# Performance work log

Hardware: AMD Instinct MI355X
Metric: run time of the kernel (lower is better)

## Reference

```python
import jax, jax.numpy as jnp
import numpy as np

B, T, C, H = 4, 2048, 1024, 16


def setup_inputs() -> dict:
    key = jax.random.key(0)
    ks = jax.random.split(key, 5)
    s_attn = 1.0 / np.sqrt(C)
    s_proj = 1.0 / np.sqrt(C)
    return {
        "x": jax.random.normal(ks[0], (B, T, C), dtype=jnp.float32),
        "w_attn": jax.random.uniform(ks[1], (3 * C, C), dtype=jnp.float32, minval=-s_attn, maxval=s_attn),
        "b_attn": jax.random.uniform(ks[2], (3 * C,), dtype=jnp.float32, minval=-s_attn, maxval=s_attn),
        "w_proj": jax.random.uniform(ks[3], (C, C), dtype=jnp.float32, minval=-s_proj, maxval=s_proj),
        "b_proj": jax.random.uniform(ks[4], (C,), dtype=jnp.float32, minval=-s_proj, maxval=s_proj),
    }


def reference(x, w_attn, b_attn, w_proj, b_proj):
    b, t, c = x.shape
    hd = c // H  # head dim
    qkv = jnp.einsum('btc,dc->btd', x, w_attn) + b_attn  # [B,T,3C]
    q, k, v = jnp.split(qkv, 3, axis=-1)
    # [B,H,T,hd]
    q = q.reshape(b, t, H, hd).transpose(0, 2, 1, 3)
    k = k.reshape(b, t, H, hd).transpose(0, 2, 1, 3)
    v = v.reshape(b, t, H, hd).transpose(0, 2, 1, 3)
    att = jnp.einsum('bhqd,bhkd->bhqk', q, k) * (1.0 / np.sqrt(hd))
    mask = jnp.tril(jnp.ones((t, t), dtype=bool))  # causal
    att = jnp.where(mask, att, -jnp.inf)
    att = jax.nn.softmax(att, axis=-1)
    y = jnp.einsum('bhqk,bhkd->bhqd', att, v)
    y = y.transpose(0, 2, 1, 3).reshape(b, t, c)
    return jnp.einsum('btc,dc->btd', y, w_proj) + b_proj
```

## Files before the change

### kernel.cpp

```cpp
#include <hip/hip_runtime.h>

#define Bb 4
#define Tt 2048
#define Cc 1024
#define Hh 16
#define NQKV 3072
#define Mtot 8192

typedef __bf16 bf16_t;
typedef unsigned short u16;
typedef __bf16 bf16x8 __attribute__((ext_vector_type(8)));
typedef __bf16 bf16x4 __attribute__((ext_vector_type(4)));
typedef short short4v __attribute__((ext_vector_type(4)));
typedef float f32x4 __attribute__((ext_vector_type(4)));
typedef float f32x16 __attribute__((ext_vector_type(16)));
typedef unsigned uint2v __attribute__((ext_vector_type(2)));

union bfu { bf16_t b; u16 u; };
union trpair { short4v h[2]; bf16x8 v; };
union pfu { unsigned u[4]; bf16x8 v; };

#define QSCALE 0.18033688011112042f

#define TRD(dst, addr, OFF)                                                     \
  asm volatile("ds_read_b64_tr_b16 %0, %1 offset:" OFF                          \
               : "=v"(dst) : "v"(addr) : "memory")

__device__ __forceinline__ unsigned cvtpk(float a, float b) {
  unsigned r;
  asm("v_cvt_pk_bf16_f32 %0, %1, %2" : "=v"(r) : "v"(a), "v"(b));
  return r;
}
__device__ __forceinline__ uint2v plswap(unsigned a, unsigned b) {
  return __builtin_amdgcn_permlane32_swap(a, b, false, false);
}

#define GLOAD16(gsrc, ldst)                                                     \
  __builtin_amdgcn_global_load_lds(                                             \
      (const __attribute__((address_space(1))) unsigned int*)(gsrc),            \
      (__attribute__((address_space(3))) unsigned int*)(ldst), 16, 0, 0)

__device__ __forceinline__ void cvt8(const float* s, u16* d, size_t i, float f) {
  float4 a = *(const float4*)(s + i);
  float4 b = *(const float4*)(s + i + 4);
  bf16x8 v;
  v[0]=(bf16_t)(a.x*f); v[1]=(bf16_t)(a.y*f); v[2]=(bf16_t)(a.z*f); v[3]=(bf16_t)(a.w*f);
  v[4]=(bf16_t)(b.x*f); v[5]=(bf16_t)(b.y*f); v[6]=(bf16_t)(b.z*f); v[7]=(bf16_t)(b.w*f);
  *(bf16x8*)(d + i) = v;
}

__global__ __launch_bounds__(256) void cvt_all(
    const float* __restrict__ x, const float* __restrict__ w_attn,
    const float* __restrict__ w_proj, const float* __restrict__ b_attn,
    u16* __restrict__ xb, u16* __restrict__ wab, u16* __restrict__ wpb,
    float* __restrict__ sbias)
{
  const int blk = blockIdx.x;
  if (blk < 4096) {
    size_t i = ((size_t)blk * 256 + threadIdx.x) * 8;
    cvt8(x, xb, i, 1.0f);
  } else if (blk < 5632) {
    size_t i = ((size_t)(blk - 4096) * 256 + threadIdx.x) * 8;
    cvt8(w_attn, wab, i, (i < (size_t)Cc * Cc) ? QSCALE : 1.0f);
  } else if (blk < 6144) {
    size_t i = ((size_t)(blk - 5632) * 256 + threadIdx.x) * 8;
    cvt8(w_proj, wpb, i, 1.0f);
  } else {
    int i0 = (blk - 6144) * 2048 + threadIdx.x * 8;
#pragma unroll
    for (int j = 0; j < 8; ++j) {
      int i = i0 + j;
      if (i < NQKV) sbias[i] = b_attn[i] * ((i < Cc) ? QSCALE : 1.0f);
    }
  }
}

__global__ __launch_bounds__(512, 2) void gemm256(
    const u16* __restrict__ A, const u16* __restrict__ Bm,
    const float* __restrict__ bias, u16* __restrict__ Cout,
    int M, int N, int K)
{
  __shared__ __attribute__((aligned(16))) u16 sa[2][8192];
  __shared__ __attribute__((aligned(16))) u16 sb[2][8192];

  const int tid  = threadIdx.x;
  const int lane = tid & 63;
  const int w    = tid >> 6;
  const int wm   = w >> 2;
  const int wn   = w & 3;
  const int l15  = lane & 15;
  const int lh   = lane >> 4;
  const int bm   = blockIdx.x * 256;
  const int bn   = blockIdx.y * 256;

  f32x4 acc[8][4] = {};

  const int sr = tid >> 2;
  const int sc = (tid & 3) * 8;
  const u16* pa0 = A  + (size_t)(bm + sr) * K + sc;
  const u16* pa1 = A  + (size_t)(bm + 128 + sr) * K + sc;
  const u16* pb0 = Bm + (size_t)(bn + sr) * K + sc;
  const u16* pb1 = Bm + (size_t)(bn + 128 + sr) * K + sc;
  const int d0 = tid * 8;

#define STAGE_T(t, p) do {                                                      \
    GLOAD16(pa0 + (size_t)(t) * 32, &sa[p][d0]);                                \
    GLOAD16(pa1 + (size_t)(t) * 32, &sa[p][d0 + 4096]);                         \
    GLOAD16(pb0 + (size_t)(t) * 32, &sb[p][d0]);                                \
    GLOAD16(pb1 + (size_t)(t) * 32, &sb[p][d0 + 4096]);                         \
  } while (0)

  const int NT = K >> 5;
  STAGE_T(0, 0);
  STAGE_T(1, 1);

  for (int t = 0; t < NT; ++t) {
    const int p = t & 1;
    if (t + 1 < NT) asm volatile("s_waitcnt vmcnt(4)" ::: "memory");
    else            asm volatile("s_waitcnt vmcnt(0)" ::: "memory");
    __builtin_amdgcn_s_barrier();
    __builtin_amdgcn_sched_barrier(0);

    bf16x8 bfr[4], afr[8];
#pragma unroll
    for (int nf = 0; nf < 4; ++nf)
      bfr[nf] = *(const bf16x8*)&sb[p][(wn*64 + nf*16 + l15) * 32 + lh*8];
#pragma unroll
    for (int mf = 0; mf < 8; ++mf)
      afr[mf] = *(const bf16x8*)&sa[p][(wm*128 + mf*16 + l15) * 32 + lh*8];

    __builtin_amdgcn_s_setprio(1);
#pragma unroll
    for (int mf = 0; mf < 8; ++mf)
#pragma unroll
      for (int nf = 0; nf < 4; ++nf)
        acc[mf][nf] = __builtin_amdgcn_mfma_f32_16x16x32_bf16(
            afr[mf], bfr[nf], acc[mf][nf], 0, 0, 0);
    __builtin_amdgcn_s_setprio(0);
    __builtin_amdgcn_sched_barrier(0);
    __builtin_amdgcn_s_barrier();
    __builtin_amdgcn_sched_barrier(0);
    if (t + 2 < NT) STAGE_T(t + 2, p);
  }
#undef STAGE_T

#pragma unroll
  for (int mf = 0; mf < 8; ++mf)
#pragma unroll
    for (int nf = 0; nf < 4; ++nf) {
      const int col = bn + wn*64 + nf*16 + l15;
      const float bs = bias[col];
#pragma unroll
      for (int r = 0; r < 4; ++r) {
        const int row = bm + wm*128 + mf*16 + lh*4 + r;
        bfu cv; cv.b = (bf16_t)(acc[mf][nf][r] + bs);
        Cout[(size_t)row * N + col] = cv.u;
      }
    }
}

template <int OUTBF16>
__global__ __launch_bounds__(256) void gemm_bf16(
    const u16* __restrict__ A, const u16* __restrict__ Bm,
    const float* __restrict__ bias, void* __restrict__ Cout,
    int M, int N, int K)
{
  __shared__ __attribute__((aligned(16))) u16 sa[128][40];
  __shared__ __attribute__((aligned(16))) u16 sb[128][40];

  const int tid  = threadIdx.x;
  const int lane = tid & 63;
  const int wid  = tid >> 6;
  const int wr   = (wid >> 1) * 64;
  const int wc   = (wid & 1) * 64;
  const int l15  = lane & 15;
  const int lh   = lane >> 4;
  const int bm   = blockIdx.x * 128;
  const int bn   = blockIdx.y * 128;

  f32x4 acc[4][4] = {};

  const int srow = tid >> 1;
  const int sseg = (tid & 1) * 16;

  const u16* pa = A  + (size_t)(bm + srow) * K + sseg;
  const u16* pb = Bm + (size_t)(bn + srow) * K + sseg;

  uint4 ar0 = *(const uint4*)pa, ar1 = *(const uint4*)(pa + 8);
  uint4 br0 = *(const uint4*)pb, br1 = *(const uint4*)(pb + 8);
  pa += 32; pb += 32;

  for (int k0 = 0; k0 < K; k0 += 32) {
    __syncthreads();
    *(uint4*)&sa[srow][sseg]     = ar0;
    *(uint4*)&sa[srow][sseg + 8] = ar1;
    *(uint4*)&sb[srow][sseg]     = br0;
    *(uint4*)&sb[srow][sseg + 8] = br1;
    __syncthreads();
    if (k0 + 32 < K) {
      ar0 = *(const uint4*)pa; ar1 = *(const uint4*)(pa + 8);
      br0 = *(const uint4*)pb; br1 = *(const uint4*)(pb + 8);
      pa += 32; pb += 32;
    }
    bf16x8 af[4], bfv[4];
#pragma unroll
    for (int mi = 0; mi < 4; mi++)
      af[mi] = *(const bf16x8*)&sa[wr + mi*16 + l15][lh * 8];
#pragma unroll
    for (int ni = 0; ni < 4; ni++)
      bfv[ni] = *(const bf16x8*)&sb[wc + ni*16 + l15][lh * 8];
#pragma unroll
    for (int mi = 0; mi < 4; mi++)
#pragma unroll
      for (int ni = 0; ni < 4; ni++)
        acc[mi][ni] = __builtin_amdgcn_mfma_f32_16x16x32_bf16(
            af[mi], bfv[ni], acc[mi][ni], 0, 0, 0);
  }

#pragma unroll
  for (int mi = 0; mi < 4; mi++) {
#pragma unroll
    for (int ni = 0; ni < 4; ni++) {
      const int col = bn + wc + ni*16 + l15;
      const float bs = bias[col];
#pragma unroll
      for (int r = 0; r < 4; r++) {
        const int row = bm + wr + mi*16 + lh*4 + r;
        const float val = acc[mi][ni][r] + bs;
        if (OUTBF16) {
          bfu cv; cv.b = (bf16_t)val;
          ((u16*)Cout)[(size_t)row * N + col] = cv.u;
        } else {
          ((float*)Cout)[(size_t)row * N + col] = val;
        }
      }
    }
  }
}

#define BUFU 9216

__global__ __launch_bounds__(512) void attn_kernel(
    const u16* __restrict__ qkv, u16* __restrict__ y)
{
  __shared__ __attribute__((aligned(16))) u16 smem[3 * BUFU];

  const int tid  = threadIdx.x;
  const int lane = tid & 63;
  const int w    = tid >> 6;
  const int l31  = lane & 31;
  const int hh   = lane >> 5;
  const int l15  = lane & 15;
  const int lh   = lane >> 4;
  const int bh   = blockIdx.y;
  const int b    = bh >> 4;
  const int head = bh & 15;

  const size_t rowbase = (size_t)b * Tt * NQKV;

  const int skey = tid >> 3;
  const int sp   = tid & 7;
  const u16* kbase = qkv + rowbase + 1024 + head*64 + sp*8;
  const u16* vbase = qkv + rowbase + 2048 + head*64 + sp*8;

  const unsigned smemB = (unsigned)(size_t)(&smem[0]);
  const unsigned trl = smemB
      + ((lh>>1)*8 + (l15>>2))*144 + (lh&1)*32 + (l15&3)*8;

  uint4 kr0, vr0;
#define LOADREGS(t) do {                                                        \
    kr0 = *(const uint4*)(kbase + (size_t)((t)*64 + skey) * NQKV);              \
    vr0 = *(const uint4*)(vbase + (size_t)((t)*64 + skey) * NQKV);              \
  } while (0)
#define STAGEB(bofs) do {                                                       \
    *(uint4*)&smem[(bofs) + skey*72 + sp*8]        = kr0;                       \
    *(uint4*)&smem[(bofs) + 4608 + skey*72 + sp*8] = vr0;                       \
  } while (0)

  for (int half = 0; half < 2; ++half) {
    const int qx    = half ? (7 - (int)blockIdx.x) : (int)blockIdx.x;
    const int qbase = qx * 256;
    const int qw    = qbase + w * 32;
    const int qi    = qw + l31;
    const int ktiles = 4*qx + 4;

    bf16x8 qfrag[4];
#pragma unroll
    for (int m = 0; m < 4; ++m)
      qfrag[m] = *(const bf16x8*)(qkv + rowbase + (size_t)qi * NQKV
                                  + head*64 + m*16 + hh*8);

    f32x16 o0 = {}, o1 = {};
    float m_run = -1e30f, l_part = 0.0f;
    f32x16 sA0, sA1, sB0, sB1;

    auto qk = [&](f32x16& t0, f32x16& t1, int kofs, int kb0) {
      f32x16 a0 = {}, a1 = {};
      __builtin_amdgcn_s_setprio(1);
#pragma unroll
      for (int m = 0; m < 4; ++m) {
        const int co = m*16 + hh*8;
        bf16x8 k0 = *(const bf16x8*)&smem[kofs + l31*72 + co];
        bf16x8 k1 = *(const bf16x8*)&smem[kofs + (32 + l31)*72 + co];
        a0 = __builtin_amdgcn_mfma_f32_32x32x16_bf16(k0, qfrag[m], a0, 0,0,0);
        a1 = __builtin_amdgcn_mfma_f32_32x32x16_bf16(k1, qfrag[m], a1, 0,0,0);
      }
      __builtin_amdgcn_s_setprio(0);
      if (kb0 + 63 > qw) {
#pragma unroll
        for (int r = 0; r < 16; ++r) {
          const int crow = (r&3) + 8*(r>>2) + 4*hh;
          if (kb0 + crow > qi)      a0[r] = -1e30f;
          if (kb0 + 32 + crow > qi) a1[r] = -1e30f;
        }
      }
      t0 = a0; t1 = a1;
    };

    auto smpv = [&](f32x16& s0, f32x16& s1, int bofs) {
      float mx[8];
#pragma unroll
      for (int i = 0; i < 8; ++i)
        mx[i] = fmaxf(fmaxf(s0[i], s0[i+8]), fmaxf(s1[i], s1[i+8]));
#pragma unroll
      for (int i = 0; i < 4; ++i) mx[i] = fmaxf(mx[i], mx[i+4]);
      mx[0] = fmaxf(mx[0], mx[2]); mx[1] = fmaxf(mx[1], mx[3]);
      float rm = fmaxf(mx[0], mx[1]);
      {
        uint2v t = plswap(__float_as_uint(rm), __float_as_uint(rm));
        rm = fmaxf(__uint_as_float(t[0]), __uint_as_float(t[1]));
      }
      if (__any(rm > m_run + 8.0f)) {
        const float mn = fmaxf(m_run, rm);
        const float al = exp2f(m_run - mn);
        m_run = mn; l_part *= al;
#pragma unroll
        for (int r = 0; r < 16; ++r) { o0[r] *= al; o1[r] *= al; }
      }

      pfu pf0, pf1, pf2, pf3;
      float lp0 = 0.f, lp1 = 0.f, lp2 = 0.f, lp3 = 0.f;
      {
        float pe[16];
#pragma unroll
        for (int r = 0; r < 16; ++r) pe[r] = exp2f(s0[r] - m_run);
#pragma unroll
        for (int r = 0; r < 4; ++r) {
          lp0 += pe[r]; lp1 += pe[4+r]; lp2 += pe[8+r]; lp3 += pe[12+r];
        }
        unsigned a0 = cvtpk(pe[0],pe[1]),  a1 = cvtpk(pe[2],pe[3]);
        unsigned a2 = cvtpk(pe[4],pe[5]),  a3 = cvtpk(pe[6],pe[7]);
        uint2v x1 = plswap(a0, a2), x2 = plswap(a1, a3);
        pf0.u[0]=x1[0]; pf0.u[1]=x2[0]; pf0.u[2]=x1[1]; pf0.u[3]=x2[1];
        unsigned b0 = cvtpk(pe[8],pe[9]),  b1 = cvtpk(pe[10],pe[11]);
        unsigned b2 = cvtpk(pe[12],pe[13]), b3 = cvtpk(pe[14],pe[15]);
        uint2v x3 = plswap(b0, b2), x4 = plswap(b1, b3);
        pf1.u[0]=x3[0]; pf1.u[1]=x4[0]; pf1.u[2]=x3[1]; pf1.u[3]=x4[1];
      }
      {
        float pe[16];
#pragma unroll
        for (int r = 0; r < 16; ++r) pe[r] = exp2f(s1[r] - m_run);
#pragma unroll
        for (int r = 0; r < 4; ++r) {
          lp0 += pe[r]; lp1 += pe[4+r]; lp2 += pe[8+r]; lp3 += pe[12+r];
        }
        unsigned a0 = cvtpk(pe[0],pe[1]),  a1 = cvtpk(pe[2],pe[3]);
        unsigned a2 = cvtpk(pe[4],pe[5]),  a3 = cvtpk(pe[6],pe[7]);
        uint2v x1 = plswap(a0, a2), x2 = plswap(a1, a3);
        pf2.u[0]=x1[0]; pf2.u[1]=x2[0]; pf2.u[2]=x1[1]; pf2.u[3]=x2[1];
        unsigned b0 = cvtpk(pe[8],pe[9]),  b1 = cvtpk(pe[10],pe[11]);
        unsigned b2 = cvtpk(pe[12],pe[13]), b3 = cvtpk(pe[14],pe[15]);
        uint2v x3 = plswap(b0, b2), x4 = plswap(b1, b3);
        pf3.u[0]=x3[0]; pf3.u[1]=x4[0]; pf3.u[2]=x3[1]; pf3.u[3]=x4[1];
      }
      l_part += (lp0 + lp1) + (lp2 + lp3);

      const unsigned va = trl + (unsigned)(bofs*2 + 9216);
      short4v ta0,tb0,ta1,tb1,ta2,tb2,ta3,tb3,ta4,tb4,ta5,tb5,ta6,tb6,ta7,tb7;
      TRD(ta0, va, "0");    TRD(tb0, va, "576");
      TRD(ta1, va, "64");   TRD(tb1, va, "640");
      TRD(ta2, va, "2304"); TRD(tb2, va, "2880");
      TRD(ta3, va, "2368"); TRD(tb3, va, "2944");
      TRD(ta4, va, "4608"); TRD(tb4, va, "5184");
      TRD(ta5, va, "4672"); TRD(tb5, va, "5248");
      TRD(ta6, va, "6912"); TRD(tb6, va, "7488");
      TRD(ta7, va, "6976"); TRD(tb7, va, "7552");
      asm volatile("s_waitcnt lgkmcnt(0)" ::: "memory");
      __builtin_amdgcn_sched_barrier(0);
      trpair v00,v01,v10,v11,v20,v21,v30,v31;
      v00.h[0]=ta0; v00.h[1]=tb0;  v01.h[0]=ta1; v01.h[1]=tb1;
      v10.h[0]=ta2; v10.h[1]=tb2;  v11.h[0]=ta3; v11.h[1]=tb3;
      v20.h[0]=ta4; v20.h[1]=tb4;  v21.h[0]=ta5; v21.h[1]=tb5;
      v30.h[0]=ta6; v30.h[1]=tb6;  v31.h[0]=ta7; v31.h[1]=tb7;
      __builtin_amdgcn_s_setprio(1);
      o0 = __builtin_amdgcn_mfma_f32_32x32x16_bf16(v00.v, pf0.v, o0, 0,0,0);
      o1 = __builtin_amdgcn_mfma_f32_32x32x16_bf16(v01.v, pf0.v, o1, 0,0,0);
      o0 = __builtin_amdgcn_mfma_f32_32x32x16_bf16(v10.v, pf1.v, o0, 0,0,0);
      o1 = __builtin_amdgcn_mfma_f32_32x32x16_bf16(v11.v, pf1.v, o1, 0,0,0);
      o0 = __builtin_amdgcn_mfma_f32_32x32x16_bf16(v20.v, pf2.v, o0, 0,0,0);
      o1 = __builtin_amdgcn_mfma_f32_32x32x16_bf16(v21.v, pf2.v, o1, 0,0,0);
      o0 = __builtin_amdgcn_mfma_f32_32x32x16_bf16(v30.v, pf3.v, o0, 0,0,0);
      o1 = __builtin_amdgcn_mfma_f32_32x32x16_bf16(v31.v, pf3.v, o1, 0,0,0);
      __builtin_amdgcn_s_setprio(0);
    };

    LOADREGS(0);
    __syncthreads();
    STAGEB(0);
    LOADREGS(1);
    __syncthreads();
    qk(sA0, sA1, 0, 0);
    STAGEB(BUFU);
    LOADREGS(2);

    int cofs = 0, nofs = BUFU, fofs = 2*BUFU;

    for (int kt = 0; kt < ktiles; kt += 2) {
      __syncthreads();
      if ((kt+1)*64 <= qw + 31) qk(sB0, sB1, nofs, (kt+1)*64);
      if (kt*64 <= qw + 31)     smpv(sA0, sA1, cofs);
      if (kt + 2 < ktiles) {
        STAGEB(fofs);
        if (kt + 3 < ktiles) LOADREGS(kt + 3);
      }
      { int t = cofs; cofs = nofs; nofs = fofs; fofs = t; }

      __syncthreads();
      if ((kt+2) < ktiles && (kt+2)*64 <= qw + 31) qk(sA0, sA1, nofs, (kt+2)*64);
      if ((kt+1)*64 <= qw + 31) smpv(sB0, sB1, cofs);
      if (kt + 3 < ktiles) {
        STAGEB(fofs);
        if (kt + 4 < ktiles) LOADREGS(kt + 4);
      }
      { int t = cofs; cofs = nofs; nofs = fofs; fofs = t; }
    }

    {
      uint2v t = plswap(__float_as_uint(l_part), __float_as_uint(l_part));
      l_part = __uint_as_float(t[0]) + __uint_as_float(t[1]);
    }
    const float inv = 1.0f / l_part;

    __syncthreads();
#pragma unroll
    for (int k4 = 0; k4 < 4; ++k4) {
      bf16x4 pa, pb;
#pragma unroll
      for (int j = 0; j < 4; ++j) {
        pa[j] = (bf16_t)(o0[4*k4 + j] * inv);
        pb[j] = (bf16_t)(o1[4*k4 + j] * inv);
      }
      *(bf16x4*)&smem[w*2304 + l31*72 +      8*k4 + 4*hh] = pa;
      *(bf16x4*)&smem[w*2304 + l31*72 + 32 + 8*k4 + 4*hh] = pb;
    }
    u16* yp = y + ((size_t)(b*Tt + qi)) * Cc + head*64;
#pragma unroll
    for (int p = 0; p < 4; ++p) {
      bf16x8 row = *(const bf16x8*)&smem[w*2304 + l31*72 + p*16 + hh*8];
      *(bf16x8*)(yp + p*16 + hh*8) = row;
    }
  }
#undef LOADREGS
#undef STAGEB
}

extern "C" void kernel_launch(void* const* d_in, const int* in_sizes, int n_in,
                              void* d_out, int out_size, void* d_ws, size_t ws_size,
                              hipStream_t stream) {
  const float* x      = (const float*)d_in[0];
  const float* w_attn = (const float*)d_in[1];
  const float* b_attn = (const float*)d_in[2];
  const float* w_proj = (const float*)d_in[3];
  const float* b_proj = (const float*)d_in[4];
  float* out = (float*)d_out;

  char* ws = (char*)d_ws;
  u16*   xb    = (u16*)(ws + 0);
  u16*   wab   = (u16*)(ws + 16777216);
  u16*   wpb   = (u16*)(ws + 23068672);
  u16*   qkvb  = (u16*)(ws + 25165824);
  u16*   yb    = (u16*)(ws + 75497472);
  float* sbias = (float*)(ws + 92274688);

  cvt_all<<<6146, 256, 0, stream>>>(x, w_attn, w_proj, b_attn,
                                    xb, wab, wpb, sbias);

  gemm256<<<dim3(Mtot/256, NQKV/256), 512, 0, stream>>>(
      xb, wab, sbias, qkvb, Mtot, NQKV, Cc);

  attn_kernel<<<dim3(4, Bb*Hh), 512, 0, stream>>>(qkvb, yb);

  gemm_bf16<0><<<dim3(Mtot/128, Cc/128), 256, 0, stream>>>(
      yb, wpb, b_proj, (void*)out, Mtot, Cc, Cc);
}
```

Measured before the change: 198.7 us.

## Restructure QKV GEMM into four-phase pipelined K=64 loop with swizzled LDS

The QKV projection GEMM now processes a K=64 step per iteration, split into four phases over two K halves and two N halves. Each phase interleaves its LDS fragment reads, the global-to-LDS staging of a future tile, and MFMA issue. Per-phase barriers and tuned vmcnt waits replace the single per-iteration barrier. LDS grows to a single 128 KB buffer with an XOR swizzle on the K-chunk column to cut bank conflicts, and occupancy drops to one block per CU. The aim is better overlap of memory loads and LDS reads with matrix math, at the cost of more barriers and lower occupancy.

```diff
diff --git a/kernel.cpp b/kernel.cpp
--- a/kernel.cpp
+++ b/kernel.cpp
@@ -75,13 +75,12 @@
   }
 }
 
-__global__ __launch_bounds__(512, 2) void gemm256(
+__global__ __launch_bounds__(512, 1) void gemm4p(
     const u16* __restrict__ A, const u16* __restrict__ Bm,
     const float* __restrict__ bias, u16* __restrict__ Cout,
     int M, int N, int K)
 {
-  __shared__ __attribute__((aligned(16))) u16 sa[2][8192];
-  __shared__ __attribute__((aligned(16))) u16 sb[2][8192];
+  __shared__ __attribute__((aligned(16))) u16 smem[65536];
 
   const int tid  = threadIdx.x;
   const int lane = tid & 63;
@@ -94,55 +93,78 @@
   const int bn   = blockIdx.y * 256;
 
   f32x4 acc[8][4] = {};
-
-  const int sr = tid >> 2;
-  const int sc = (tid & 3) * 8;
-  const u16* pa0 = A  + (size_t)(bm + sr) * K + sc;
-  const u16* pa1 = A  + (size_t)(bm + 128 + sr) * K + sc;
-  const u16* pb0 = Bm + (size_t)(bn + sr) * K + sc;
-  const u16* pb1 = Bm + (size_t)(bn + 128 + sr) * K + sc;
-  const int d0 = tid * 8;
-
-#define STAGE_T(t, p) do {                                                      \
-    GLOAD16(pa0 + (size_t)(t) * 32, &sa[p][d0]);                                \
-    GLOAD16(pa1 + (size_t)(t) * 32, &sa[p][d0 + 4096]);                         \
-    GLOAD16(pb0 + (size_t)(t) * 32, &sb[p][d0]);                                \
-    GLOAD16(pb1 + (size_t)(t) * 32, &sb[p][d0 + 4096]);                         \
+  bf16x8 af[8], bf0, bf1;
+
+  const int sc8 = (((tid & 3) ^ ((tid >> 3) & 3))) * 8;
+  const u16* gA = A  + (size_t)(bm + (tid >> 2)) * K + sc8;
+  const u16* gB = Bm + (size_t)(bn + (tid >> 2)) * K + sc8;
+  const size_t rj = (size_t)128 * K;
+
+  const int xs = (lh ^ ((l15 >> 1) & 3)) * 8;
+
+#define SAo(p,kd) ((p)*16384 + (kd)*8192)
+#define SBo(p,kd) (32768 + (p)*16384 + (kd)*8192)
+#define STAGE_A(p,kd,t) do {                                                    \
+    GLOAD16(gA +      (size_t)(t)*64 + (kd)*32, &smem[SAo(p,kd) + tid*8]);      \
+    GLOAD16(gA + rj + (size_t)(t)*64 + (kd)*32, &smem[SAo(p,kd) + 4096 + tid*8]);\
   } while (0)
-
-  const int NT = K >> 5;
-  STAGE_T(0, 0);
-  STAGE_T(1, 1);
+#define STAGE_B(p,kd,t) do {                                                    \
+    GLOAD16(gB +      (size_t)(t)*64 + (kd)*32, &smem[SBo(p,kd) + tid*8]);      \
+    GLOAD16(gB + rj + (size_t)(t)*64 + (kd)*32, &smem[SBo(p,kd) + 4096 + tid*8]);\
+  } while (0)
+
+  const int NT = K >> 6;
+
+  STAGE_A(0,0,0); STAGE_B(0,0,0);
+  STAGE_A(0,1,0); STAGE_B(0,1,0);
+  STAGE_A(1,0,1); STAGE_B(1,0,1);
+  asm volatile("s_waitcnt vmcnt(8)" ::: "memory");
+  __builtin_amdgcn_s_barrier();
+  __builtin_amdgcn_sched_barrier(0);
+
+  auto phase = [&](int p, int kd, int nh, auto stagefn, int vm) {
+    if (nh == 0) {
+#pragma unroll
+      for (int mf = 0; mf < 8; ++mf)
+        af[mf] = *(const bf16x8*)&smem[SAo(p,kd) + (wm*128 + mf*16 + l15)*32 + xs];
+    }
+    bf0 = *(const bf16x8*)&smem[SBo(p,kd) + (wn*64 + (nh*2+0)*16 + l15)*32 + xs];
+    bf1 = *(const bf16x8*)&smem[SBo(p,kd) + (wn*64 + (nh*2+1)*16 + l15)*32 + xs];
+    stagefn();
+    __builtin_amdgcn_sched_barrier(0);
+    __builtin_amdgcn_s_barrier();
+    asm volatile("s_waitcnt lgkmcnt(0)" ::: "memory");
+    __builtin_amdgcn_sched_barrier(0);
+    __builtin_amdgcn_s_setprio(1);
+#pragma unroll
+    for (int mf = 0; mf < 8; ++mf) {
+      acc[mf][nh*2+0] = __builtin_amdgcn_mfma_f32_16x16x32_bf16(
+          af[mf], bf0, acc[mf][nh*2+0], 0, 0, 0);
+      acc[mf][nh*2+1] = __builtin_amdgcn_mfma_f32_16x16x32_bf16(
+          af[mf], bf1, acc[mf][nh*2+1], 0, 0, 0);
+    }
+    __builtin_amdgcn_s_setprio(0);
+    __builtin_amdgcn_sched_barrier(0);
+    if (vm == 8)      asm volatile("s_waitcnt vmcnt(8)" ::: "memory");
+    else if (vm == 4) asm volatile("s_waitcnt vmcnt(4)" ::: "memory");
+    else if (vm == 0) asm volatile("s_waitcnt vmcnt(0)" ::: "memory");
+    __builtin_amdgcn_s_barrier();
+    __builtin_amdgcn_sched_barrier(0);
+  };
 
   for (int t = 0; t < NT; ++t) {
     const int p = t & 1;
-    if (t + 1 < NT) asm volatile("s_waitcnt vmcnt(4)" ::: "memory");
-    else            asm volatile("s_waitcnt vmcnt(0)" ::: "memory");
-    __builtin_amdgcn_s_barrier();
-    __builtin_amdgcn_sched_barrier(0);
-
-    bf16x8 bfr[4], afr[8];
-#pragma unroll
-    for (int nf = 0; nf < 4; ++nf)
-      bfr[nf] = *(const bf16x8*)&sb[p][(wn*64 + nf*16 + l15) * 32 + lh*8];
-#pragma unroll
-    for (int mf = 0; mf < 8; ++mf)
-      afr[mf] = *(const bf16x8*)&sa[p][(wm*128 + mf*16 + l15) * 32 + lh*8];
-
-    __builtin_amdgcn_s_setprio(1);
-#pragma unroll
-    for (int mf = 0; mf < 8; ++mf)
-#pragma unroll
-      for (int nf = 0; nf < 4; ++nf)
-        acc[mf][nf] = __builtin_amdgcn_mfma_f32_16x16x32_bf16(
-            afr[mf], bfr[nf], acc[mf][nf], 0, 0, 0);
-    __builtin_amdgcn_s_setprio(0);
-    __builtin_amdgcn_sched_barrier(0);
-    __builtin_amdgcn_s_barrier();
-    __builtin_amdgcn_sched_barrier(0);
-    if (t + 2 < NT) STAGE_T(t + 2, p);
+    phase(p, 0, 0, [&]{ if (t+1 < NT) STAGE_A(1-p, 1, t+1); }, -1);
+    phase(p, 0, 1, [&]{ if (t+1 < NT) STAGE_B(1-p, 1, t+1); },
+          (t < NT-1) ? 8 : 0);
+    phase(p, 1, 0, [&]{ if (t+2 < NT) STAGE_A(p, 0, t+2); }, -1);
+    phase(p, 1, 1, [&]{ if (t+2 < NT) STAGE_B(p, 0, t+2); },
+          (t < NT-2) ? 8 : ((t == NT-2) ? 4 : 0));
   }
-#undef STAGE_T
+#undef STAGE_A
+#undef STAGE_B
+#undef SAo
+#undef SBo
 
 #pragma unroll
   for (int mf = 0; mf < 8; ++mf)
@@ -486,7 +508,7 @@
   cvt_all<<<6146, 256, 0, stream>>>(x, w_attn, w_proj, b_attn,
                                     xb, wab, wpb, sbias);
 
-  gemm256<<<dim3(Mtot/256, NQKV/256), 512, 0, stream>>>(
+  gemm4p<<<dim3(Mtot/256, NQKV/256), 512, 0, stream>>>(
       xb, wab, sbias, qkvb, Mtot, NQKV, Cc);
 
   attn_kernel<<<dim3(4, Bb*Hh), 512, 0, stream>>>(qkvb, yb);
```

After: 183.2 us. 1.08x faster.
